# Kernel tuning notes

Measured on AMD Instinct MI355X. Metric: run time of the kernel, lower is better.

The kernel has to match this reference:

```python
import jax, jax.numpy as jnp
import numpy as np


def _rope_tables(T, d):
    half = d // 2
    i = jnp.arange(half, dtype=jnp.float32)
    theta = 10000.0 ** (-2.0 * i / d)          # [half]
    m = jnp.arange(T, dtype=jnp.float32)[:, None]  # [T,1]
    ang = m * theta[None, :]                    # [T,half]
    return jnp.cos(ang), jnp.sin(ang)


def _rotate(v, cos, sin):
    # interleaved even/odd RoPE rotation, vectorized
    B, T, d = v.shape
    half = d // 2
    v2 = v.reshape(B, T, half, 2)
    even, odd = v2[..., 0], v2[..., 1]
    c = cos[None, :, :]
    s = sin[None, :, :]
    new_even = even * c - odd * s
    new_odd = even * s + odd * c
    return jnp.stack([new_even, new_odd], axis=-1).reshape(B, T, d)


def setup_inputs() -> dict:
    key = jax.random.key(0)
    k1, k2, k3, k4 = jax.random.split(key, 4)
    B, T, d = 4, 2048, 1024
    x = jax.random.normal(k1, (B, T, d), dtype=jnp.float32)
    scale = 0.02
    Wq = jax.random.normal(k2, (d, d), dtype=jnp.float32) * scale
    Wk = jax.random.normal(k3, (d, d), dtype=jnp.float32) * scale
    Wv = jax.random.normal(k4, (d, d), dtype=jnp.float32) * scale
    return {"x": x, "Wq": Wq, "Wk": Wk, "Wv": Wv}


def reference(x, Wq, Wk, Wv):
    B, T, d = x.shape
    cos, sin = _rope_tables(T, d)
    # torch Linear: y = x @ W.T
    Q = jnp.einsum('btd,ed->bte', x, Wq)
    K = jnp.einsum('btd,ed->bte', x, Wk)
    V = jnp.einsum('btd,ed->bte', x, Wv)
    Qr = _rotate(Q, cos, sin)
    Kr = _rotate(K, cos, sin)
    scores = jnp.einsum('bqd,bkd->bqk', Qr, Kr) / jnp.sqrt(jnp.float32(d))
    # NOTE: original uses tril with diagonal=1 (allows one future position)
    mask = jnp.tril(jnp.ones((T, T), dtype=bool), k=1)
    scores = jnp.where(mask[None, :, :], scores, -jnp.inf)
    attn = jax.nn.softmax(scores, axis=-1)
    out = jnp.einsum('bqk,bkd->bqd', attn, V)
    return out
```

## Files before the change

### kernel.cpp

```cpp
#include <hip/hip_runtime.h>


typedef float f32x4 __attribute__((ext_vector_type(4)));
typedef __bf16 bf16x8 __attribute__((ext_vector_type(8)));

#define BM 128
#define BN 128
#define BK 64

__device__ __forceinline__ unsigned short f2bf(float f) {
  union { float f; unsigned int u; } c; c.f = f;
  unsigned int u = c.u;
  u += 0x7fffu + ((u >> 16) & 1u);
  return (unsigned short)(u >> 16);
}
__device__ __forceinline__ float bf2f(unsigned short h) {
  union { unsigned int u; float f; } c; c.u = ((unsigned int)h) << 16;
  return c.f;
}

__device__ __forceinline__ void async16(const unsigned short* gp, unsigned short* lp) {
  __builtin_amdgcn_global_load_lds(
      (const __attribute__((address_space(1))) void*)gp,
      (__attribute__((address_space(3))) void*)lp, 16, 0, 0);
}

__global__ __launch_bounds__(256) void cvt_all(
    const float4* __restrict__ x, const float4* __restrict__ wq,
    const float4* __restrict__ wk, const float4* __restrict__ wv,
    ushort4* __restrict__ xb, ushort4* __restrict__ wb,
    float4* __restrict__ rowsums) {
  int b = blockIdx.x, t = threadIdx.x;
  if (b == 11264) {
#pragma unroll
    for (int i = 0; i < 8; ++i) rowsums[i * 256 + t] = float4{0.f, 0.f, 0.f, 0.f};
    return;
  }
  const float4* src;
  ushort4* dst;
  long i;
  if (b < 8192) { src = x; dst = xb; i = (long)b * 256 + t; }
  else if (b < 9216) { src = wq; dst = wb; i = (long)(b - 8192) * 256 + t; }
  else if (b < 10240) { src = wk; dst = wb + 262144; i = (long)(b - 9216) * 256 + t; }
  else { src = wv; dst = wb + 524288; i = (long)(b - 10240) * 256 + t; }
  float4 v = src[i];
  ushort4 o;
  o.x = f2bf(v.x); o.y = f2bf(v.y); o.z = f2bf(v.z); o.w = f2bf(v.w);
  dst[i] = o;
}

__device__ __forceinline__ void gemm_body(
    const unsigned short* __restrict__ A, const unsigned short* __restrict__ B,
    unsigned short* As, unsigned short* Bs,
    int lda, int ldb, int m0, int n0, int ktiles,
    int tid, int lane, int wave, f32x4 acc[4][4]) {
  const int wm = (wave >> 1) * 64;
  const int wn = (wave & 1) * 64;
  const int fm = lane & 15;
  const int q = lane >> 4;

  long goffA[4], goffB[4];
#pragma unroll
  for (int p = 0; p < 4; ++p) {
    int f = p * 256 + tid;
    int row = f >> 3;
    int c = (f & 7) ^ (row & 7);
    goffA[p] = (long)(m0 + row) * lda + c * 8;
    goffB[p] = (long)(n0 + row) * ldb + c * 8;
  }

  for (int kt = 0; kt < ktiles; ++kt) {
    const long k0 = (long)kt * BK;
    __syncthreads();
#pragma unroll
    for (int p = 0; p < 4; ++p) {
      async16(A + goffA[p] + k0, As + (p * 256 + tid) * 8);
      async16(B + goffB[p] + k0, Bs + (p * 256 + tid) * 8);
    }
    __syncthreads();

#pragma unroll
    for (int s = 0; s < 2; ++s) {
      bf16x8 af[4], bfr[4];
#pragma unroll
      for (int i = 0; i < 4; ++i) {
        int row = wm + i * 16 + fm;
        af[i] = *(const bf16x8*)&As[row * 64 + ((((s << 2) | q) ^ (row & 7)) << 3)];
      }
#pragma unroll
      for (int j = 0; j < 4; ++j) {
        int row = wn + j * 16 + fm;
        bfr[j] = *(const bf16x8*)&Bs[row * 64 + ((((s << 2) | q) ^ (row & 7)) << 3)];
      }
#pragma unroll
      for (int i = 0; i < 4; ++i)
#pragma unroll
        for (int j = 0; j < 4; ++j)
          acc[i][j] = __builtin_amdgcn_mfma_f32_16x16x32_bf16(af[i], bfr[j], acc[i][j], 0, 0, 0);
    }
  }
}

__global__ __launch_bounds__(256) void qkv_rope_gemm(
    const unsigned short* __restrict__ A, const unsigned short* __restrict__ B,
    unsigned short* __restrict__ Qr, unsigned short* __restrict__ Kr,
    unsigned short* __restrict__ Vt) {
  __shared__ __align__(16) unsigned short As[BM * BK];
  __shared__ __align__(16) unsigned short Bs[BN * BK];
  const int tid = threadIdx.x, lane = tid & 63, wave = tid >> 6;
  const int bm = blockIdx.x, bn = blockIdx.y;
  const int m0 = bm * BM, n0 = bn * BN;
  const int wm = (wave >> 1) * 64, wn = (wave & 1) * 64;
  const int q = lane >> 4, fm = lane & 15;

  f32x4 acc[4][4];
#pragma unroll
  for (int i = 0; i < 4; ++i)
#pragma unroll
    for (int j = 0; j < 4; ++j) acc[i][j] = (f32x4)(0.f);

  gemm_body(A, B, As, Bs, 1024, 1024, m0, n0, 16, tid, lane, wave, acc);

  if (n0 < 2048) {
    const float NEG = -13.287712379549449f / 1024.f;
    unsigned short* dst = (n0 < 1024) ? Qr : Kr;
    const int t00 = (m0 + wm + q * 4) & 2047;
#pragma unroll
    for (int j = 0; j < 4; ++j) {
      int c = (n0 & 1023) + wn + j * 16 + fm;
      float th = exp2f((float)(c & ~1) * NEG);
      float sgn = (c & 1) ? 1.f : -1.f;
      float ang0 = (float)t00 * th;
      float cb = __cosf(ang0), sb = __sinf(ang0);
      float c1 = __cosf(th), s1 = __sinf(th);
      float c16 = __cosf(16.f * th), s16 = __sinf(16.f * th);
#pragma unroll
      for (int i = 0; i < 4; ++i) {
        int gmB = m0 + wm + i * 16 + q * 4;
        float cr = cb, sr = sb;
#pragma unroll
        for (int r = 0; r < 4; ++r) {
          float v = acc[i][j][r];
          float p = __shfl_xor(v, 1);
          dst[(long)(gmB + r) * 1024 + c] = f2bf(v * cr + sgn * p * sr);
          float crn = cr * c1 - sr * s1;
          sr = sr * c1 + cr * s1;
          cr = crn;
        }
        float cbn = cb * c16 - sb * s16;
        sb = sb * c16 + cb * s16;
        cb = cbn;
      }
    }
  } else {
    const int c0 = n0 - 2048;
#pragma unroll
    for (int j = 0; j < 4; ++j) {
      int c = c0 + wn + j * 16 + fm;
#pragma unroll
      for (int i = 0; i < 4; ++i) {
        int gmB = m0 + wm + i * 16 + q * 4;
        int b = gmB >> 11, t = gmB & 2047;
        ushort4 pk;
        pk.x = f2bf(acc[i][j][0]);
        pk.y = f2bf(acc[i][j][1]);
        pk.z = f2bf(acc[i][j][2]);
        pk.w = f2bf(acc[i][j][3]);
        *(ushort4*)&Vt[((long)b * 1024 + c) * 2048 + t] = pk;
      }
    }
  }
}

__global__ __launch_bounds__(256) void s_gemm(
    const unsigned short* __restrict__ Qr, const unsigned short* __restrict__ Kr,
    unsigned short* __restrict__ Sb, float* __restrict__ rowsums) {
  __shared__ __align__(16) unsigned short As[BM * BK];
  __shared__ __align__(16) unsigned short Bs[BN * BK];
  const int tid = threadIdx.x, lane = tid & 63, wave = tid >> 6;
  const int bm = blockIdx.y, bn = blockIdx.x, z = blockIdx.z;
  if (bn > bm + 1) return;
  const unsigned short* A = Qr + (long)z * 2048 * 1024;
  const unsigned short* B = Kr + (long)z * 2048 * 1024;
  unsigned short* S = Sb + (long)z * 2048 * 2048;
  float* rs = rowsums + (long)z * 2048;
  const int m0 = bm * BM, n0 = bn * BN;
  const int wm = (wave >> 1) * 64, wn = (wave & 1) * 64;
  const int q = lane >> 4, fm = lane & 15;

  f32x4 acc[4][4];
#pragma unroll
  for (int i = 0; i < 4; ++i)
#pragma unroll
    for (int j = 0; j < 4; ++j) acc[i][j] = (f32x4)(0.f);

  gemm_body(A, B, As, Bs, 1024, 1024, m0, n0, 16, tid, lane, wave, acc);

  float* rsum = (float*)Bs;
  __syncthreads();
  if (tid < 128) rsum[tid] = 0.f;
  __syncthreads();

#pragma unroll
  for (int i = 0; i < 4; ++i) {
    int gmB = m0 + wm + i * 16 + q * 4;
    float ps[4] = {0.f, 0.f, 0.f, 0.f};
#pragma unroll
    for (int j = 0; j < 4; ++j) {
      int gn = n0 + wn + j * 16 + fm;
#pragma unroll
      for (int r = 0; r < 4; ++r) {
        float e = (gn <= gmB + r + 1) ? __expf(acc[i][j][r] * 0.03125f) : 0.f;
        unsigned short h = f2bf(e);
        S[(long)(gmB + r) * 2048 + gn] = h;
        ps[r] += bf2f(h);
      }
    }
#pragma unroll
    for (int r = 0; r < 4; ++r) {
      float v = ps[r];
      v += __shfl_xor(v, 1);
      v += __shfl_xor(v, 2);
      v += __shfl_xor(v, 4);
      v += __shfl_xor(v, 8);
      if (fm == 0) atomicAdd(&rsum[wm + i * 16 + q * 4 + r], v);
    }
  }
  __syncthreads();
  if (tid < 128) atomicAdd(&rs[m0 + tid], rsum[tid]);
}

__global__ __launch_bounds__(256) void pv_gemm(
    const unsigned short* __restrict__ Sb, const unsigned short* __restrict__ Vt,
    const float* __restrict__ rowsums, float* __restrict__ out, int b0) {
  __shared__ __align__(16) unsigned short As[BM * BK];
  __shared__ __align__(16) unsigned short Bs[BN * BK];
  const int tid = threadIdx.x, lane = tid & 63, wave = tid >> 6;
  const int bm = blockIdx.y, bn = blockIdx.x, z = blockIdx.z;
  const unsigned short* A = Sb + (long)z * 2048 * 2048;
  const unsigned short* B = Vt + (long)(b0 + z) * 1024 * 2048;
  const float* rs = rowsums + (long)(b0 + z) * 2048;
  float* C = out + (long)(b0 + z) * 2048 * 1024;
  int ktiles = 2 * bm + 3;
  if (ktiles > 32) ktiles = 32;
  const int m0 = bm * BM, n0 = bn * BN;
  const int wm = (wave >> 1) * 64, wn = (wave & 1) * 64;
  const int q = lane >> 4, fm = lane & 15;

  f32x4 acc[4][4];
#pragma unroll
  for (int i = 0; i < 4; ++i)
#pragma unroll
    for (int j = 0; j < 4; ++j) acc[i][j] = (f32x4)(0.f);

  gemm_body(A, B, As, Bs, 2048, 2048, m0, n0, ktiles, tid, lane, wave, acc);

#pragma unroll
  for (int i = 0; i < 4; ++i) {
    int gmB = m0 + wm + i * 16 + q * 4;
#pragma unroll
    for (int r = 0; r < 4; ++r) {
      float inv = 1.f / rs[gmB + r];
#pragma unroll
      for (int j = 0; j < 4; ++j) {
        int gn = n0 + wn + j * 16 + fm;
        C[(long)(gmB + r) * 1024 + gn] = acc[i][j][r] * inv;
      }
    }
  }
}

extern "C" void kernel_launch(void* const* d_in, const int* in_sizes, int n_in,
                              void* d_out, int out_size, void* d_ws, size_t ws_size,
                              hipStream_t stream) {
  const float* x = (const float*)d_in[0];
  const float* Wq = (const float*)d_in[1];
  const float* Wk = (const float*)d_in[2];
  const float* Wv = (const float*)d_in[3];
  float* out = (float*)d_out;

  float* rowsums = (float*)d_ws;
  unsigned short* Qr = (unsigned short*)d_ws + 16384;
  unsigned short* Kr = Qr + (long)8192 * 1024;
  unsigned short* Vt = Kr + (long)8192 * 1024;
  unsigned short* xb = Vt + (long)8192 * 1024;
  unsigned short* Wb = xb + (long)8192 * 1024;
  unsigned short* Sb = xb;

  int BCH = 4;
  while (BCH > 1 && (size_t)32768 + (size_t)(48 + 8 * BCH) * 1024 * 1024 > ws_size)
    BCH >>= 1;

  cvt_all<<<11265, 256, 0, stream>>>((const float4*)x, (const float4*)Wq,
                                     (const float4*)Wk, (const float4*)Wv,
                                     (ushort4*)xb, (ushort4*)Wb, (float4*)rowsums);

  qkv_rope_gemm<<<dim3(64, 24), 256, 0, stream>>>(xb, Wb, Qr, Kr, Vt);

  for (int b0 = 0; b0 < 4; b0 += BCH) {
    s_gemm<<<dim3(16, 16, BCH), 256, 0, stream>>>(Qr + (long)b0 * 2048 * 1024,
                                                  Kr + (long)b0 * 2048 * 1024,
                                                  Sb, rowsums + (long)b0 * 2048);
    pv_gemm<<<dim3(8, 16, BCH), 256, 0, stream>>>(Sb, Vt, rowsums, out, b0);
  }
}
```

Baseline: 252.7 us.

## Double-buffer LDS tiles in GEMM body and compact causal tile launches

Shared GEMM loop now double-buffers the A/B LDS tiles and prefetches the next K tile via async global-to-LDS loads while the current one feeds MFMAs, using explicit vmcnt waits and barriers. s_gemm launches only the 151 lower-triangular(+1) tiles per batch instead of early-exiting blocks. pv_gemm reverses row order so the longest-K rows are scheduled first. LDS use per block doubles, which may reduce occupancy.

```diff
diff --git a/kernel.cpp b/kernel.cpp
--- a/kernel.cpp
+++ b/kernel.cpp
@@ -7,6 +7,7 @@
 #define BM 128
 #define BN 128
 #define BK 64
+#define TILE (BM * BK)
 
 __device__ __forceinline__ unsigned short f2bf(float f) {
   union { float f; unsigned int u; } c; c.f = f;
@@ -69,15 +70,29 @@
     goffB[p] = (long)(n0 + row) * ldb + c * 8;
   }
 
+#pragma unroll
+  for (int p = 0; p < 4; ++p) {
+    async16(A + goffA[p], As + (p * 256 + tid) * 8);
+    async16(B + goffB[p], Bs + (p * 256 + tid) * 8);
+  }
+
   for (int kt = 0; kt < ktiles; ++kt) {
-    const long k0 = (long)kt * BK;
-    __syncthreads();
-#pragma unroll
-    for (int p = 0; p < 4; ++p) {
-      async16(A + goffA[p] + k0, As + (p * 256 + tid) * 8);
-      async16(B + goffB[p] + k0, Bs + (p * 256 + tid) * 8);
-    }
-    __syncthreads();
+    const int cur = (kt & 1) * TILE;
+    const int nxt = ((kt + 1) & 1) * TILE;
+
+    asm volatile("s_barrier" ::: "memory");
+    if (kt + 1 < ktiles) {
+      const long k0 = (long)(kt + 1) * BK;
+#pragma unroll
+      for (int p = 0; p < 4; ++p) {
+        async16(A + goffA[p] + k0, As + nxt + (p * 256 + tid) * 8);
+        async16(B + goffB[p] + k0, Bs + nxt + (p * 256 + tid) * 8);
+      }
+      asm volatile("s_waitcnt vmcnt(8)" ::: "memory");
+    } else {
+      asm volatile("s_waitcnt vmcnt(0)" ::: "memory");
+    }
+    asm volatile("s_barrier" ::: "memory");
 
 #pragma unroll
     for (int s = 0; s < 2; ++s) {
@@ -85,12 +100,12 @@
 #pragma unroll
       for (int i = 0; i < 4; ++i) {
         int row = wm + i * 16 + fm;
-        af[i] = *(const bf16x8*)&As[row * 64 + ((((s << 2) | q) ^ (row & 7)) << 3)];
+        af[i] = *(const bf16x8*)&As[cur + row * 64 + ((((s << 2) | q) ^ (row & 7)) << 3)];
       }
 #pragma unroll
       for (int j = 0; j < 4; ++j) {
         int row = wn + j * 16 + fm;
-        bfr[j] = *(const bf16x8*)&Bs[row * 64 + ((((s << 2) | q) ^ (row & 7)) << 3)];
+        bfr[j] = *(const bf16x8*)&Bs[cur + row * 64 + ((((s << 2) | q) ^ (row & 7)) << 3)];
       }
 #pragma unroll
       for (int i = 0; i < 4; ++i)
@@ -105,8 +120,8 @@
     const unsigned short* __restrict__ A, const unsigned short* __restrict__ B,
     unsigned short* __restrict__ Qr, unsigned short* __restrict__ Kr,
     unsigned short* __restrict__ Vt) {
-  __shared__ __align__(16) unsigned short As[BM * BK];
-  __shared__ __align__(16) unsigned short Bs[BN * BK];
+  __shared__ __align__(16) unsigned short As[2 * TILE];
+  __shared__ __align__(16) unsigned short Bs[2 * TILE];
   const int tid = threadIdx.x, lane = tid & 63, wave = tid >> 6;
   const int bm = blockIdx.x, bn = blockIdx.y;
   const int m0 = bm * BM, n0 = bn * BN;
@@ -175,11 +190,18 @@
 __global__ __launch_bounds__(256) void s_gemm(
     const unsigned short* __restrict__ Qr, const unsigned short* __restrict__ Kr,
     unsigned short* __restrict__ Sb, float* __restrict__ rowsums) {
-  __shared__ __align__(16) unsigned short As[BM * BK];
-  __shared__ __align__(16) unsigned short Bs[BN * BK];
+  __shared__ __align__(16) unsigned short As[2 * TILE];
+  __shared__ __align__(16) unsigned short Bs[2 * TILE];
   const int tid = threadIdx.x, lane = tid & 63, wave = tid >> 6;
-  const int bm = blockIdx.y, bn = blockIdx.x, z = blockIdx.z;
-  if (bn > bm + 1) return;
+  const int z = blockIdx.z;
+  int idx = blockIdx.x, bm = 0;
+#pragma unroll 1
+  for (; bm < 16; ++bm) {
+    int cnt = (bm + 2 > 16) ? 16 : bm + 2;
+    if (idx < cnt) break;
+    idx -= cnt;
+  }
+  const int bn = idx;
   const unsigned short* A = Qr + (long)z * 2048 * 1024;
   const unsigned short* B = Kr + (long)z * 2048 * 1024;
   unsigned short* S = Sb + (long)z * 2048 * 2048;
@@ -233,10 +255,10 @@
 __global__ __launch_bounds__(256) void pv_gemm(
     const unsigned short* __restrict__ Sb, const unsigned short* __restrict__ Vt,
     const float* __restrict__ rowsums, float* __restrict__ out, int b0) {
-  __shared__ __align__(16) unsigned short As[BM * BK];
-  __shared__ __align__(16) unsigned short Bs[BN * BK];
+  __shared__ __align__(16) unsigned short As[2 * TILE];
+  __shared__ __align__(16) unsigned short Bs[2 * TILE];
   const int tid = threadIdx.x, lane = tid & 63, wave = tid >> 6;
-  const int bm = blockIdx.y, bn = blockIdx.x, z = blockIdx.z;
+  const int bm = 15 - blockIdx.y, bn = blockIdx.x, z = blockIdx.z;
   const unsigned short* A = Sb + (long)z * 2048 * 2048;
   const unsigned short* B = Vt + (long)(b0 + z) * 1024 * 2048;
   const float* rs = rowsums + (long)(b0 + z) * 2048;
@@ -298,7 +320,7 @@
   qkv_rope_gemm<<<dim3(64, 24), 256, 0, stream>>>(xb, Wb, Qr, Kr, Vt);
 
   for (int b0 = 0; b0 < 4; b0 += BCH) {
-    s_gemm<<<dim3(16, 16, BCH), 256, 0, stream>>>(Qr + (long)b0 * 2048 * 1024,
+    s_gemm<<<dim3(151, 1, BCH), 256, 0, stream>>>(Qr + (long)b0 * 2048 * 1024,
                                                   Kr + (long)b0 * 2048 * 1024,
                                                   Sb, rowsums + (long)b0 * 2048);
     pv_gemm<<<dim3(8, 16, BCH), 256, 0, stream>>>(Sb, Vt, rowsums, out, b0);
```

Measured after the change: 249.1 us. Within noise of the previous version (-1.4%).
